# Kernel optimization log

Measured on AMD Instinct MI355X. Metric: run time of the kernel, lower is better.

## Reference

```python
import jax, jax.numpy as jnp
import numpy as np

HEADS = 16
D_MODEL = 1024


def setup_inputs() -> dict:
    key = jax.random.key(0)
    ks = jax.random.split(key, 12)
    B, S, D = 4, 2048, D_MODEL
    s = 1.0 / np.sqrt(D)
    return {
        "q": jax.random.normal(ks[0], (B, S, D), jnp.float32),
        "k": jax.random.normal(ks[1], (B, S, D), jnp.float32),
        "v": jax.random.normal(ks[2], (B, S, D), jnp.float32),
        "mask": jnp.ones((B, S, S), jnp.int32),
        "W_q": jax.random.normal(ks[3], (D, D), jnp.float32) * s,
        "b_q": jnp.zeros((D,), jnp.float32),
        "W_k": jax.random.normal(ks[4], (D, D), jnp.float32) * s,
        "b_k": jnp.zeros((D,), jnp.float32),
        "W_v": jax.random.normal(ks[5], (D, D), jnp.float32) * s,
        "b_v": jnp.zeros((D,), jnp.float32),
        "W_o": jax.random.normal(ks[6], (D, D), jnp.float32) * s,
        "b_o": jnp.zeros((D,), jnp.float32),
    }


def reference(q, k, v, mask, W_q, b_q, W_k, b_k, W_v, b_v, W_o, b_o):
    B, Sq, D = q.shape
    H = HEADS
    d_k = D // H
    # torch Linear: x @ W.T + b
    qh = (q @ W_q.T + b_q).reshape(B, Sq, H, d_k).transpose(0, 2, 1, 3)
    kh = (k @ W_k.T + b_k).reshape(B, -1, H, d_k).transpose(0, 2, 1, 3)
    vh = (v @ W_v.T + b_v).reshape(B, -1, H, d_k).transpose(0, 2, 1, 3)
    scores = jnp.einsum("bhqd,bhkd->bhqk", qh, kh) / jnp.sqrt(jnp.float32(d_k))
    scores = jnp.where(mask[:, None, :, :] == 0, -jnp.inf, scores)
    attn = jax.nn.softmax(scores, axis=-1)
    out = jnp.einsum("bhqk,bhkd->bhqd", attn, vh)
    out = out.transpose(0, 2, 1, 3).reshape(B, Sq, D)
    return out @ W_o.T + b_o
```

## Files before the change

kernel.cpp:

```cpp
#include <hip/hip_runtime.h>
#include <hip/hip_bf16.h>
#include <cmath>
#include <cstddef>

#define B_  4
#define S_  2048
#define D_  1024
#define H_  16
#define DK_ 64
#define M_  (B_*S_)
#define MB(x) ((size_t)(x) << 20)

typedef unsigned short u16;
typedef __attribute__((ext_vector_type(8))) short s16x8;
typedef __attribute__((ext_vector_type(8))) unsigned short u16x8;
typedef __attribute__((ext_vector_type(4))) unsigned short u16x4;
typedef __attribute__((ext_vector_type(4))) float f32x4;
typedef __attribute__((ext_vector_type(4))) unsigned int u32x4;

typedef __attribute__((address_space(3))) char as3char;
typedef __attribute__((address_space(1))) const char as1char;

__device__ inline u16 f2bf(float f) {
  unsigned int u = __float_as_uint(f);
  u += 0x7fffu + ((u >> 16) & 1u);
  return (u16)(u >> 16);
}
__device__ inline float bf2f(u16 h) {
  return __uint_as_float(((unsigned int)h) << 16);
}

__device__ inline size_t tsw(int m, int k) {
  int row = m & 127, kk = k & 63;
  return ((size_t)((m >> 7) * 16 + (k >> 6)) << 14)
       + (size_t)(((row * 128 + (kk >> 3) * 16) ^ ((row & 7) << 4)) + (kk & 7) * 2);
}

__global__ __launch_bounds__(256)
void pack_mask(const int* __restrict__ mask, unsigned long long* __restrict__ Mp)
{
  int w    = blockIdx.x * 4 + (threadIdx.x >> 6);
  int lane = threadIdx.x & 63;
  int m = mask[(size_t)w * 64 + lane];
  unsigned long long bits = __ballot(m != 0);
  if (lane == 0) Mp[w] = bits;
}

__global__ __launch_bounds__(256)
void split_w_t(const float* __restrict__ W, u16* __restrict__ hi,
               u16* __restrict__ lo)
{
  int id = blockIdx.x * 256 + threadIdx.x;
  int n  = id >> 7;
  int k8 = (id & 127) << 3;
  const float* p = W + (size_t)n * 1024 + k8;
  float4 x0 = *(const float4*)p;
  float4 x1 = *(const float4*)(p + 4);
  float xs[8] = {x0.x, x0.y, x0.z, x0.w, x1.x, x1.y, x1.z, x1.w};
  u16x8 h, l;
#pragma unroll
  for (int e = 0; e < 8; ++e) {
    u16 hh = f2bf(xs[e]);
    h[e] = hh;
    l[e] = f2bf(xs[e] - bf2f(hh));
  }
  size_t byte = tsw(n, k8);
  *(u16x8*)((char*)hi + byte) = h;
  *(u16x8*)((char*)lo + byte) = l;
}

__global__ __launch_bounds__(256)
void cvt3(const float* __restrict__ a, const float* __restrict__ b,
          const float* __restrict__ c, u16* __restrict__ oa,
          u16* __restrict__ ob, u16* __restrict__ oc)
{
  const float* src = blockIdx.z == 0 ? a : (blockIdx.z == 1 ? b : c);
  u16*         dst = blockIdx.z == 0 ? oa : (blockIdx.z == 1 ? ob : oc);
  int id = blockIdx.x * 256 + threadIdx.x;
  int m  = id >> 7;
  int k8 = (id & 127) << 3;
  const float* p = src + (size_t)m * 1024 + k8;
  float4 x0 = *(const float4*)p;
  float4 x1 = *(const float4*)(p + 4);
  u16x8 px;
  px[0]=f2bf(x0.x); px[1]=f2bf(x0.y); px[2]=f2bf(x0.z); px[3]=f2bf(x0.w);
  px[4]=f2bf(x1.x); px[5]=f2bf(x1.y); px[6]=f2bf(x1.z); px[7]=f2bf(x1.w);
  *(u16x8*)((char*)dst + tsw(m, k8)) = px;
}

__global__ __launch_bounds__(256)
void proj_gemm_qkv(const u16* __restrict__ qb, const u16* __restrict__ kb,
                   const u16* __restrict__ vb, const u16* __restrict__ Wqb,
                   const u16* __restrict__ Wkb, const u16* __restrict__ Wvb,
                   const float* __restrict__ bq, const float* __restrict__ bk,
                   const float* __restrict__ bv, u16* __restrict__ oq,
                   u16* __restrict__ ok, u16* __restrict__ ov)
{
  __shared__ __align__(16) u16 smem[16384];
  char* const sX = (char*)smem;
  char* const sW = (char*)smem + 16384;

  const int z = blockIdx.z;
  const u16* Xb = z == 0 ? qb : (z == 1 ? kb : vb);
  const u16* Wb = z == 0 ? Wqb : (z == 1 ? Wkb : Wvb);
  const float* bias = z == 0 ? bq : (z == 1 ? bk : bv);
  u16* out = z == 0 ? oq : (z == 1 ? ok : ov);
  const float scale = z == 0 ? 0.125f : 1.0f;

  const int tid  = threadIdx.x;
  const int lane = tid & 63, wid = tid >> 6;
  const int l15  = lane & 15, l4 = lane >> 4;
  const int wm = (wid >> 1) * 64, wn = (wid & 1) * 64;
  const int mb = blockIdx.x, nb = blockIdx.y;

  f32x4 acc[4][4];
#pragma unroll
  for (int i = 0; i < 4; ++i)
#pragma unroll
    for (int j = 0; j < 4; ++j)
      acc[i][j] = f32x4{0.f, 0.f, 0.f, 0.f};

  const char* xsrc = (const char*)Xb + ((size_t)(mb * 16) << 14) + wid * 4096 + lane * 16;
  const char* wsrc = (const char*)Wb + ((size_t)(nb * 16) << 14) + wid * 4096 + lane * 16;

  for (int kbi = 0; kbi < 16; ++kbi) {
#pragma unroll
    for (int i = 0; i < 4; ++i) {
      __builtin_amdgcn_global_load_lds((const as1char*)(xsrc + i * 1024),
                                       (as3char*)(sX + wid * 4096 + i * 1024), 16, 0, 0);
      __builtin_amdgcn_global_load_lds((const as1char*)(wsrc + i * 1024),
                                       (as3char*)(sW + wid * 4096 + i * 1024), 16, 0, 0);
    }
    xsrc += 16384; wsrc += 16384;
    __syncthreads();

#pragma unroll
    for (int kc = 0; kc < 2; ++kc) {
      s16x8 af[4], bf[4];
#pragma unroll
      for (int i = 0; i < 4; ++i) {
        int ar = wm + i * 16 + l15;
        af[i] = *(const s16x8*)(sX + ((ar * 128 + kc * 64 + l4 * 16) ^ ((ar & 7) << 4)));
        int br = wn + i * 16 + l15;
        bf[i] = *(const s16x8*)(sW + ((br * 128 + kc * 64 + l4 * 16) ^ ((br & 7) << 4)));
      }
#pragma unroll
      for (int i = 0; i < 4; ++i)
#pragma unroll
        for (int j = 0; j < 4; ++j)
          acc[i][j] = __builtin_amdgcn_mfma_f32_16x16x32_bf16(af[i], bf[j], acc[i][j], 0, 0, 0);
    }
    __syncthreads();
  }

  float bj[4];
#pragma unroll
  for (int j = 0; j < 4; ++j) bj[j] = bias[nb * 128 + wn + j * 16 + l15];

#pragma unroll
  for (int i = 0; i < 4; ++i) {
#pragma unroll
    for (int r = 0; r < 4; ++r) {
      int mm = mb * 128 + wm + i * 16 + l4 * 4 + r;
      int bb = mm >> 11, s = mm & (S_ - 1);
#pragma unroll
      for (int j = 0; j < 4; ++j) {
        int n = nb * 128 + wn + j * 16 + l15;
        int hh = n >> 6, d = n & 63;
        u16 val = f2bf((acc[i][j][r] + bj[j]) * scale);
        if (z == 0) {
          out[(((size_t)bb * H_ + hh) * S_ + s) * DK_ + d] = val;
        } else if (z == 1) {
          size_t base = (((size_t)bb * H_ + hh) * 32 + (s >> 6)) * 8192;
          int r2 = s & 63;
          *(u16*)((char*)out + base
                  + (((r2 * 128 + (d >> 3) * 16) ^ ((r2 & 7) << 4)) + (d & 7) * 2)) = val;
        } else {
          size_t base = (((size_t)bb * H_ + hh) * 32 + (s >> 6)) * 8192;
          int kk2 = s & 63;
          int slot = ((kk2 >> 5) * 4 + ((kk2 >> 2) & 3) + d) & 7;
          *(u16*)((char*)out + base
                  + d * 128 + slot * 16 + ((kk2 >> 4) & 1) * 8 + (kk2 & 3) * 2) = val;
        }
      }
    }
  }
}

__global__ __launch_bounds__(256)
void proj_out_t(const u16* __restrict__ Xhi, const u16* __restrict__ Xlo,
                const u16* __restrict__ Whi, const u16* __restrict__ Wlo,
                const float* __restrict__ bias, float* __restrict__ out)
{
  __shared__ __align__(16) u16 smem[32768];
  char* const sXh = (char*)smem;
  char* const sXl = (char*)smem + 16384;
  char* const sWh = (char*)smem + 32768;
  char* const sWl = (char*)smem + 49152;

  const int tid  = threadIdx.x;
  const int lane = tid & 63, wid = tid >> 6;
  const int l15  = lane & 15, l4 = lane >> 4;
  const int wm = (wid >> 1) * 64, wn = (wid & 1) * 64;
  const int mb = blockIdx.x, nb = blockIdx.y;

  f32x4 acc[4][4];
#pragma unroll
  for (int i = 0; i < 4; ++i)
#pragma unroll
    for (int j = 0; j < 4; ++j)
      acc[i][j] = f32x4{0.f, 0.f, 0.f, 0.f};

  const int toff = wid * 4096 + lane * 16;
  const char* xh = (const char*)Xhi + ((size_t)(mb * 16) << 14) + toff;
  const char* xl = (const char*)Xlo + ((size_t)(mb * 16) << 14) + toff;
  const char* wh = (const char*)Whi + ((size_t)(nb * 16) << 14) + toff;
  const char* wl = (const char*)Wlo + ((size_t)(nb * 16) << 14) + toff;

  for (int kb = 0; kb < 16; ++kb) {
#pragma unroll
    for (int i = 0; i < 4; ++i) {
      __builtin_amdgcn_global_load_lds((const as1char*)(xh + i * 1024),
                                       (as3char*)(sXh + wid * 4096 + i * 1024), 16, 0, 0);
      __builtin_amdgcn_global_load_lds((const as1char*)(xl + i * 1024),
                                       (as3char*)(sXl + wid * 4096 + i * 1024), 16, 0, 0);
      __builtin_amdgcn_global_load_lds((const as1char*)(wh + i * 1024),
                                       (as3char*)(sWh + wid * 4096 + i * 1024), 16, 0, 0);
      __builtin_amdgcn_global_load_lds((const as1char*)(wl + i * 1024),
                                       (as3char*)(sWl + wid * 4096 + i * 1024), 16, 0, 0);
    }
    xh += 16384; xl += 16384; wh += 16384; wl += 16384;
    __syncthreads();

#pragma unroll
    for (int kc = 0; kc < 2; ++kc) {
      s16x8 ah[4], al[4], bh[4], bl[4];
#pragma unroll
      for (int i = 0; i < 4; ++i) {
        int ar = wm + i * 16 + l15;
        int aoff = (ar * 128 + kc * 64 + l4 * 16) ^ ((ar & 7) << 4);
        ah[i] = *(const s16x8*)(sXh + aoff);
        al[i] = *(const s16x8*)(sXl + aoff);
        int br = wn + i * 16 + l15;
        int boff = (br * 128 + kc * 64 + l4 * 16) ^ ((br & 7) << 4);
        bh[i] = *(const s16x8*)(sWh + boff);
        bl[i] = *(const s16x8*)(sWl + boff);
      }
#pragma unroll
      for (int i = 0; i < 4; ++i)
#pragma unroll
        for (int j = 0; j < 4; ++j) {
          acc[i][j] = __builtin_amdgcn_mfma_f32_16x16x32_bf16(ah[i], bh[j], acc[i][j], 0, 0, 0);
          acc[i][j] = __builtin_amdgcn_mfma_f32_16x16x32_bf16(ah[i], bl[j], acc[i][j], 0, 0, 0);
          acc[i][j] = __builtin_amdgcn_mfma_f32_16x16x32_bf16(al[i], bh[j], acc[i][j], 0, 0, 0);
        }
    }
    __syncthreads();
  }

  float bj[4];
#pragma unroll
  for (int j = 0; j < 4; ++j) bj[j] = bias[nb * 128 + wn + j * 16 + l15];

#pragma unroll
  for (int i = 0; i < 4; ++i) {
#pragma unroll
    for (int r = 0; r < 4; ++r) {
      int mm = mb * 128 + wm + i * 16 + l4 * 4 + r;
#pragma unroll
      for (int j = 0; j < 4; ++j) {
        int n = nb * 128 + wn + j * 16 + l15;
        out[(size_t)mm * D_ + n] = acc[i][j][r] + bj[j];
      }
    }
  }
}

__global__ __launch_bounds__(512)
void flash_attn_mfma9(const u16* __restrict__ Qh, const char* __restrict__ Kimg,
                      const char* __restrict__ Vimg,
                      const unsigned long long* __restrict__ Mp,
                      u16* __restrict__ AOhi, u16* __restrict__ AOlo)
{
  __shared__ __align__(16) char smem[32768];
  char* const sK0 = smem;
  char* const sV0 = smem + 8192;
  char* const sK1 = smem + 16384;
  char* const sV1 = smem + 24576;

  const int tid  = threadIdx.x;
  const int lane = tid & 63, wid = tid >> 6;
  const int l15  = lane & 15, l4 = lane >> 4;

  const int wgid = blockIdx.x + (blockIdx.y << 4);
  const int bh   = (wgid & 7) * 8 + (wgid >> 7);
  const int qt   = (wgid >> 3) & 15;
  const int b = bh >> 4, h = bh & 15;
  const int q0 = qt * 128;
  const int qw = q0 + wid * 16;
  const int myq = qw + l15;

  const float L2E = 1.4426950408889634f;
  const float SH  = 12.0f * L2E;

  const u16* qbase = Qh + ((size_t)bh * S_ + myq) * DK_;
  s16x8 qf[2];
  qf[0] = *(const s16x8*)(qbase + l4 * 8);
  qf[1] = *(const s16x8*)(qbase + 32 + l4 * 8);

  const char* kimg = Kimg + (size_t)bh * 32 * 8192 + tid * 16;
  const char* vimg = Vimg + (size_t)bh * 32 * 8192 + tid * 16;
  const int ldst = wid * 1024;

  const int kswz = (l15 & 7) << 4;
  const int kcol = l4 * 16;
  const int vs0  = ((l4 + l15) & 7) * 16;
  const int vs1  = ((4 + l4 + l15) & 7) * 16;

  const unsigned long long* mrow = Mp + ((size_t)b * S_ + myq) * (S_ / 64);

  s16x8 onesf;
#pragma unroll
  for (int e = 0; e < 8; ++e) onesf[e] = (short)0x3F80;

  f32x4 o[4];
#pragma unroll
  for (int n = 0; n < 4; ++n) o[n] = f32x4{0.f, 0.f, 0.f, 0.f};
  f32x4 ol = f32x4{0.f, 0.f, 0.f, 0.f};

  auto stage = [&](char* sKd, char* sVd, int t) {
    __builtin_amdgcn_global_load_lds((const as1char*)(kimg + (size_t)t * 8192),
                                     (as3char*)(sKd + ldst), 16, 0, 0);
    __builtin_amdgcn_global_load_lds((const as1char*)(vimg + (size_t)t * 8192),
                                     (as3char*)(sVd + ldst), 16, 0, 0);
  };

  auto compute_tile = [&](const char* sKc, const char* sVc,
                          unsigned long long mbits) {
    f32x4 sc[4];
    __builtin_amdgcn_s_setprio(1);
#pragma unroll
    for (int n = 0; n < 4; ++n) {
      sc[n] = f32x4{0.f, 0.f, 0.f, 0.f};
#pragma unroll
      for (int kc = 0; kc < 2; ++kc) {
        int row = n * 16 + l15;
        s16x8 kf = *(const s16x8*)(sKc + ((row * 128 + kc * 64 + kcol) ^ kswz));
        sc[n] = __builtin_amdgcn_mfma_f32_16x16x32_bf16(kf, qf[kc], sc[n], 0, 0, 0);
      }
    }
    __builtin_amdgcn_s_setprio(0);

    if (!__all(mbits == 0xFFFFFFFFFFFFFFFFull)) {
#pragma unroll
      for (int n = 0; n < 4; ++n) {
        unsigned mb2 = (unsigned)(mbits >> (n * 16 + l4 * 4)) & 15u;
#pragma unroll
        for (int r = 0; r < 4; ++r)
          if (!((mb2 >> r) & 1u)) sc[n][r] = -INFINITY;
      }
    }

    float p[4][4];
#pragma unroll
    for (int n = 0; n < 4; ++n)
#pragma unroll
      for (int r = 0; r < 4; ++r)
        p[n][r] = __builtin_amdgcn_exp2f(fmaf(sc[n][r], L2E, -SH));

    s16x8 pf[2];
#pragma unroll
    for (int kc = 0; kc < 2; ++kc) {
      unsigned r0, r1, r2, r3;
      asm("v_cvt_pk_bf16_f32 %0, %1, %2" : "=v"(r0) : "v"(p[2*kc][0]),   "v"(p[2*kc][1]));
      asm("v_cvt_pk_bf16_f32 %0, %1, %2" : "=v"(r1) : "v"(p[2*kc][2]),   "v"(p[2*kc][3]));
      asm("v_cvt_pk_bf16_f32 %0, %1, %2" : "=v"(r2) : "v"(p[2*kc+1][0]), "v"(p[2*kc+1][1]));
      asm("v_cvt_pk_bf16_f32 %0, %1, %2" : "=v"(r3) : "v"(p[2*kc+1][2]), "v"(p[2*kc+1][3]));
      u32x4 uu = {r0, r1, r2, r3};
      pf[kc] = __builtin_bit_cast(s16x8, uu);
    }

    __builtin_amdgcn_s_setprio(1);
#pragma unroll
    for (int kc = 0; kc < 2; ++kc) {
      ol = __builtin_amdgcn_mfma_f32_16x16x32_bf16(pf[kc], onesf, ol, 0, 0, 0);
#pragma unroll
      for (int n = 0; n < 4; ++n) {
        s16x8 vf = *(const s16x8*)(sVc + n * 2048 + l15 * 128 + (kc ? vs1 : vs0));
        o[n] = __builtin_amdgcn_mfma_f32_16x16x32_bf16(pf[kc], vf, o[n], 0, 0, 0);
      }
    }
    __builtin_amdgcn_s_setprio(0);
  };

  unsigned long long mb_next = mrow[0];
  stage(sK0, sV0, 0);
  __syncthreads();

  for (int t = 0; t < S_ / 64; t += 2) {
    if (t + 1 < S_ / 64) stage(sK1, sV1, t + 1);
    unsigned long long mbits = mb_next;
    if (t + 1 < S_ / 64) mb_next = mrow[t + 1];
    compute_tile(sK0, sV0, mbits);
    __syncthreads();

    if (t + 2 < S_ / 64) stage(sK0, sV0, t + 2);
    mbits = mb_next;
    if (t + 2 < S_ / 64) mb_next = mrow[t + 2];
    compute_tile(sK1, sV1, mbits);
    __syncthreads();
  }

  float linv[4];
#pragma unroll
  for (int r = 0; r < 4; ++r)
    linv[r] = ol[r] > 0.f ? 1.f / ol[r] : 0.f;
#pragma unroll
  for (int n = 0; n < 4; ++n)
#pragma unroll
    for (int r = 0; r < 4; ++r) {
      float val = o[n][r] * linv[r];
      u16 hh = f2bf(val);
      int m = b * S_ + qw + l4 * 4 + r;
      int k = h * 64 + n * 16 + l15;
      size_t byte = tsw(m, k);
      *(u16*)((char*)AOhi + byte) = hh;
      *(u16*)((char*)AOlo + byte) = f2bf(val - bf2f(hh));
    }
}

extern "C" void kernel_launch(void* const* d_in, const int* in_sizes, int n_in,
                              void* d_out, int out_size, void* d_ws, size_t ws_size,
                              hipStream_t stream)
{
  const float* q    = (const float*)d_in[0];
  const float* k    = (const float*)d_in[1];
  const float* v    = (const float*)d_in[2];
  const int*   mask = (const int*)  d_in[3];
  const float* Wq   = (const float*)d_in[4];
  const float* bq   = (const float*)d_in[5];
  const float* Wk   = (const float*)d_in[6];
  const float* bk   = (const float*)d_in[7];
  const float* Wv   = (const float*)d_in[8];
  const float* bv   = (const float*)d_in[9];
  const float* Wo   = (const float*)d_in[10];
  const float* bo   = (const float*)d_in[11];
  float* out = (float*)d_out;

  char* ws = (char*)d_ws;
  u16*  Qh   = (u16*)(ws);
  char* Kimg = ws + MB(16);
  char* Vimg = ws + MB(32);
  u16*  AOhi = (u16*)(ws + MB(48));
  u16*  AOlo = (u16*)(ws + MB(64));
  u16*  Whi  = (u16*)(ws + MB(80));
  u16*  Wlo  = (u16*)(ws + MB(82));
  unsigned long long* Mp = (unsigned long long*)(ws + MB(84));
  u16* kb2  = (u16*)(ws + MB(48));
  u16* qb2  = (u16*)(ws + MB(64));
  u16* vb2  = (u16*)(ws + MB(86));
  u16* Wqb  = (u16*)(ws + MB(102));
  u16* Wkb  = (u16*)(ws + MB(104));
  u16* Wvb  = (u16*)(ws + MB(106));

  dim3 tblk(256);

  cvt3<<<dim3(4096, 1, 3), tblk, 0, stream>>>(q, k, v, qb2, kb2, vb2);
  cvt3<<<dim3(512, 1, 3), tblk, 0, stream>>>(Wq, Wk, Wv, Wqb, Wkb, Wvb);
  pack_mask<<<dim3((B_ * S_ * (S_ / 64)) / 4), tblk, 0, stream>>>(mask, Mp);
  split_w_t<<<dim3(512), tblk, 0, stream>>>(Wo, Whi, Wlo);

  proj_gemm_qkv<<<dim3(M_ / 128, D_ / 128, 3), tblk, 0, stream>>>(
      qb2, kb2, vb2, Wqb, Wkb, Wvb, bq, bk, bv,
      Qh, (u16*)Kimg, (u16*)Vimg);

  dim3 gattn(S_ / 128, B_ * H_);
  flash_attn_mfma9<<<gattn, dim3(512), 0, stream>>>(Qh, Kimg, Vimg, Mp, AOhi, AOlo);

  proj_out_t<<<dim3(M_ / 128, D_ / 128), tblk, 0, stream>>>(AOhi, AOlo, Whi, Wlo, bo, out);
}
```

Measured before the change: 278.8 us.

## Enlarge QKV projection tile to 256x128 with 512 threads; merge weight prep kernels

The QKV projection GEMM now uses 512-thread blocks computing 256x128 output tiles. Each W tile loaded into LDS is therefore reused across twice as many rows, which halves weight-tile global traffic and the block count. LDS use per block grows to 48 KB, which may reduce occupancy. Separately, the Wq/Wk/Wv bf16 conversion and the Wo hi/lo split are merged into one launch to cut kernel launch overhead.

```diff
diff --git a/kernel.cpp b/kernel.cpp
--- a/kernel.cpp
+++ b/kernel.cpp
@@ -47,26 +47,39 @@
 }
 
 __global__ __launch_bounds__(256)
-void split_w_t(const float* __restrict__ W, u16* __restrict__ hi,
-               u16* __restrict__ lo)
-{
+void prep_w(const float* __restrict__ Wq, const float* __restrict__ Wk,
+            const float* __restrict__ Wv, const float* __restrict__ Wo,
+            u16* __restrict__ oWq, u16* __restrict__ oWk,
+            u16* __restrict__ oWv, u16* __restrict__ oWhi,
+            u16* __restrict__ oWlo)
+{
+  const int z = blockIdx.z;
   int id = blockIdx.x * 256 + threadIdx.x;
   int n  = id >> 7;
   int k8 = (id & 127) << 3;
-  const float* p = W + (size_t)n * 1024 + k8;
+  const float* src = z == 0 ? Wq : (z == 1 ? Wk : (z == 2 ? Wv : Wo));
+  const float* p = src + (size_t)n * 1024 + k8;
   float4 x0 = *(const float4*)p;
   float4 x1 = *(const float4*)(p + 4);
   float xs[8] = {x0.x, x0.y, x0.z, x0.w, x1.x, x1.y, x1.z, x1.w};
-  u16x8 h, l;
-#pragma unroll
-  for (int e = 0; e < 8; ++e) {
-    u16 hh = f2bf(xs[e]);
-    h[e] = hh;
-    l[e] = f2bf(xs[e] - bf2f(hh));
+  size_t byte = tsw(n, k8);
+  if (z < 3) {
+    u16* dst = z == 0 ? oWq : (z == 1 ? oWk : oWv);
+    u16x8 px;
+#pragma unroll
+    for (int e = 0; e < 8; ++e) px[e] = f2bf(xs[e]);
+    *(u16x8*)((char*)dst + byte) = px;
+  } else {
+    u16x8 h, l;
+#pragma unroll
+    for (int e = 0; e < 8; ++e) {
+      u16 hh = f2bf(xs[e]);
+      h[e] = hh;
+      l[e] = f2bf(xs[e] - bf2f(hh));
+    }
+    *(u16x8*)((char*)oWhi + byte) = h;
+    *(u16x8*)((char*)oWlo + byte) = l;
   }
-  size_t byte = tsw(n, k8);
-  *(u16x8*)((char*)hi + byte) = h;
-  *(u16x8*)((char*)lo + byte) = l;
 }
 
 __global__ __launch_bounds__(256)
@@ -88,7 +101,7 @@
   *(u16x8*)((char*)dst + tsw(m, k8)) = px;
 }
 
-__global__ __launch_bounds__(256)
+__global__ __launch_bounds__(512)
 void proj_gemm_qkv(const u16* __restrict__ qb, const u16* __restrict__ kb,
                    const u16* __restrict__ vb, const u16* __restrict__ Wqb,
                    const u16* __restrict__ Wkb, const u16* __restrict__ Wvb,
@@ -96,9 +109,9 @@
                    const float* __restrict__ bv, u16* __restrict__ oq,
                    u16* __restrict__ ok, u16* __restrict__ ov)
 {
-  __shared__ __align__(16) u16 smem[16384];
+  __shared__ __align__(16) u16 smem[24576];
   char* const sX = (char*)smem;
-  char* const sW = (char*)smem + 16384;
+  char* const sW = (char*)smem + 32768;
 
   const int z = blockIdx.z;
   const u16* Xb = z == 0 ? qb : (z == 1 ? kb : vb);
@@ -110,7 +123,7 @@
   const int tid  = threadIdx.x;
   const int lane = tid & 63, wid = tid >> 6;
   const int l15  = lane & 15, l4 = lane >> 4;
-  const int wm = (wid >> 1) * 64, wn = (wid & 1) * 64;
+  const int wm = (wid & 3) * 64, wn = (wid >> 2) * 64;
   const int mb = blockIdx.x, nb = blockIdx.y;
 
   f32x4 acc[4][4];
@@ -120,18 +133,23 @@
     for (int j = 0; j < 4; ++j)
       acc[i][j] = f32x4{0.f, 0.f, 0.f, 0.f};
 
-  const char* xsrc = (const char*)Xb + ((size_t)(mb * 16) << 14) + wid * 4096 + lane * 16;
-  const char* wsrc = (const char*)Wb + ((size_t)(nb * 16) << 14) + wid * 4096 + lane * 16;
+  const char* xbase = (const char*)Xb + ((size_t)(mb * 32) << 14) + tid * 16;
+  const char* wbase = (const char*)Wb + ((size_t)(nb * 16) << 14) + tid * 16;
+  const int xh = wm >> 7;
 
   for (int kbi = 0; kbi < 16; ++kbi) {
 #pragma unroll
-    for (int i = 0; i < 4; ++i) {
-      __builtin_amdgcn_global_load_lds((const as1char*)(xsrc + i * 1024),
-                                       (as3char*)(sX + wid * 4096 + i * 1024), 16, 0, 0);
-      __builtin_amdgcn_global_load_lds((const as1char*)(wsrc + i * 1024),
-                                       (as3char*)(sW + wid * 4096 + i * 1024), 16, 0, 0);
-    }
-    xsrc += 16384; wsrc += 16384;
+    for (int r = 0; r < 4; ++r) {
+      const char* g = xbase + (((size_t)((r >> 1) * 16 + kbi)) << 14) + (r & 1) * 8192;
+      __builtin_amdgcn_global_load_lds((const as1char*)g,
+                                       (as3char*)(sX + r * 8192 + tid * 16), 16, 0, 0);
+    }
+#pragma unroll
+    for (int r = 0; r < 2; ++r) {
+      const char* g = wbase + (((size_t)kbi) << 14) + r * 8192;
+      __builtin_amdgcn_global_load_lds((const as1char*)g,
+                                       (as3char*)(sW + r * 8192 + tid * 16), 16, 0, 0);
+    }
     __syncthreads();
 
 #pragma unroll
@@ -139,8 +157,9 @@
       s16x8 af[4], bf[4];
 #pragma unroll
       for (int i = 0; i < 4; ++i) {
-        int ar = wm + i * 16 + l15;
-        af[i] = *(const s16x8*)(sX + ((ar * 128 + kc * 64 + l4 * 16) ^ ((ar & 7) << 4)));
+        int ar = (wm & 127) + i * 16 + l15;
+        af[i] = *(const s16x8*)(sX + xh * 16384
+                 + ((ar * 128 + kc * 64 + l4 * 16) ^ ((ar & 7) << 4)));
         int br = wn + i * 16 + l15;
         bf[i] = *(const s16x8*)(sW + ((br * 128 + kc * 64 + l4 * 16) ^ ((br & 7) << 4)));
       }
@@ -161,7 +180,7 @@
   for (int i = 0; i < 4; ++i) {
 #pragma unroll
     for (int r = 0; r < 4; ++r) {
-      int mm = mb * 128 + wm + i * 16 + l4 * 4 + r;
+      int mm = mb * 256 + wm + i * 16 + l4 * 4 + r;
       int bb = mm >> 11, s = mm & (S_ - 1);
 #pragma unroll
       for (int j = 0; j < 4; ++j) {
@@ -466,11 +485,11 @@
   dim3 tblk(256);
 
   cvt3<<<dim3(4096, 1, 3), tblk, 0, stream>>>(q, k, v, qb2, kb2, vb2);
-  cvt3<<<dim3(512, 1, 3), tblk, 0, stream>>>(Wq, Wk, Wv, Wqb, Wkb, Wvb);
+  prep_w<<<dim3(512, 1, 4), tblk, 0, stream>>>(Wq, Wk, Wv, Wo,
+                                               Wqb, Wkb, Wvb, Whi, Wlo);
   pack_mask<<<dim3((B_ * S_ * (S_ / 64)) / 4), tblk, 0, stream>>>(mask, Mp);
-  split_w_t<<<dim3(512), tblk, 0, stream>>>(Wo, Whi, Wlo);
-
-  proj_gemm_qkv<<<dim3(M_ / 128, D_ / 128, 3), tblk, 0, stream>>>(
+
+  proj_gemm_qkv<<<dim3(M_ / 256, D_ / 128, 3), dim3(512), 0, stream>>>(
       qb2, kb2, vb2, Wqb, Wkb, Wvb, bq, bk, bv,
       Qh, (u16*)Kimg, (u16*)Vimg);
 
```

Result: no change. 273.6 us (-1.9%).
